# Kernel optimization log

Measured on AMD Instinct MI355X. Metric: run time of the kernel, lower is better.

The kernel has to match this reference:

```python
import jax, jax.numpy as jnp
import numpy as np

N_IMG = 1024
N_VIEWS = 90


def _bilinear(img, yi, xi):
    """Bilinear sample img at float coords (yi=row, xi=col); 0 outside (skimage warp cval=0)."""
    n = img.shape[0]
    y0 = jnp.floor(yi)
    x0 = jnp.floor(xi)
    wy = yi - y0
    wx = xi - x0
    y0i = y0.astype(jnp.int32)
    x0i = x0.astype(jnp.int32)

    def get(yy, xx):
        valid = (yy >= 0) & (yy < n) & (xx >= 0) & (xx < n)
        v = img[jnp.clip(yy, 0, n - 1), jnp.clip(xx, 0, n - 1)]
        return jnp.where(valid, v, jnp.zeros((), img.dtype))

    v00 = get(y0i, x0i)
    v01 = get(y0i, x0i + 1)
    v10 = get(y0i + 1, x0i)
    v11 = get(y0i + 1, x0i + 1)
    return (v00 * (1 - wy) * (1 - wx) + v01 * (1 - wy) * wx
            + v10 * wy * (1 - wx) + v11 * wy * wx)


def radon_jax(image, theta_deg):
    """skimage.transform.radon(image, theta, circle=True) equivalent.
    Rotate image by each angle (bilinear, about center = N//2, inverse map as in
    skimage warp) and sum over rows. Returns sinogram [N, n_angles]."""
    n = image.shape[0]
    center = n // 2
    ang = jnp.deg2rad(theta_deg.astype(image.dtype))
    cos_a = jnp.cos(ang)  # [A]
    sin_a = jnp.sin(ang)
    coords = jnp.arange(n, dtype=image.dtype)
    X, Y = jnp.meshgrid(coords, coords)  # X = col (x), Y = row (y), [N, N]

    def rotate_and_sum(ca, sa):
        # inverse map: src = R @ dst (homogeneous, (x, y) order) as in skimage radon
        x_in = ca * X + sa * Y - center * (ca + sa - 1)
        y_in = -sa * X + ca * Y - center * (ca - sa - 1)
        rotated = _bilinear(image, y_in, x_in)  # [N, N]
        return rotated.sum(axis=0)  # sum over rows -> projection [N]

    sino = jax.vmap(rotate_and_sum)(cos_a, sin_a)  # [A, N]
    return sino.T  # [N, A] to match skimage radon layout


def setup_inputs() -> dict:
    key = jax.random.key(0)
    k1, _ = jax.random.split(key)
    x = jax.random.normal(k1, (N_IMG, N_IMG), dtype=jnp.float32)
    theta = jnp.arange(N_VIEWS, dtype=jnp.float32) * 2.0  # 0..178 deg, 2-deg spacing
    return {"x": x, "theta": theta}


def reference(x, theta):
    return radon_jax(x, theta)
```

## Files before the change

kernel.cpp:

```cpp
#include <hip/hip_runtime.h>

#define N_IMG    1024
#define N_VIEWS  90
#define CENTER   512
#define NTHREADS 512
#define NWAVES   8
#define JOBS     4
#define PIT      96
#define BUFW     9088

typedef float v2f __attribute__((ext_vector_type(2)));

__device__ __forceinline__ void map_coords(float ca, float sa, float cx, float cy,
                                           float Xf, float Yf,
                                           float& x_in, float& y_in) {
    const float fx0 = fmaf(ca, Xf, cx);
    const float fy0 = fmaf(-sa, Xf, cy);
    x_in = fmaf(sa, Yf, fx0);
    y_in = fmaf(ca, Yf, fy0);
}

__device__ __forceinline__ void gload_lds4(const float* g, float* l) {
    __builtin_amdgcn_global_load_lds((const __attribute__((address_space(1))) void*)g,
                                     (__attribute__((address_space(3))) void*)l, 4, 0, 0);
}
__device__ __forceinline__ void gload_lds16(const float* g, float* l) {
    __builtin_amdgcn_global_load_lds((const __attribute__((address_space(1))) void*)g,
                                     (__attribute__((address_space(3))) void*)l, 16, 0, 0);
}

__global__ __launch_bounds__(256) void prep(const float* __restrict__ img,
                                            float* __restrict__ T,
                                            const float* __restrict__ theta,
                                            float* __restrict__ prm) {
    if (blockIdx.x == 256) {
        const int a = threadIdx.x;
        if (a < N_VIEWS) {
            const float ang = theta[a] * 0.017453292519943295f;
            double sd_, cd_;
            sincos((double)ang, &sd_, &cd_);
            const float s0 = (float)sd_, c0 = (float)cd_;
            const float cx0 = (float)CENTER * (1.0f - c0 - s0);
            const float cy0 = (float)CENTER * (1.0f - c0 + s0);
            float c, s, cx, cy, fl;
            if (fabsf(s0) > fabsf(c0)) {
                c = s0; s = -c0; cx = 1023.0f - cy0; cy = cx0; fl = 1.0f;
            } else {
                c = c0; s = s0;  cx = cx0;            cy = cy0;  fl = 0.0f;
            }
            float* p = prm + (a << 3);
            p[0] = c; p[1] = s; p[2] = cx; p[3] = cy; p[4] = fl;
        }
        return;
    }
    __shared__ float tile[64][65];
    const int t  = blockIdx.x, tr = t >> 4, tc = t & 15;
    const int tid = threadIdx.x, lane = tid & 63, w = tid >> 6;
    #pragma unroll
    for (int k = 0; k < 16; ++k) {
        const int row = (w << 4) + k;
        tile[row][lane] = img[(size_t)((tr << 6) + row) * N_IMG + (tc << 6) + lane];
    }
    __syncthreads();
    #pragma unroll
    for (int k = 0; k < 16; ++k) {
        const int j = (tc << 6) + (w << 4) + k;
        const int i = 1023 - ((tr << 6) + lane);
        T[(size_t)j * N_IMG + i] = tile[lane][(w << 4) + k];
    }
}

__global__ __launch_bounds__(NTHREADS, 8) void radon_fused(const float* __restrict__ img,
                                                           const float* __restrict__ Tbuf,
                                                           const float* __restrict__ theta,
                                                           const float* __restrict__ prm,
                                                           float* __restrict__ out,
                                                           int useT) {
    __shared__ float buf[BUFW];

    const int tx = blockIdx.x;
    const int q  = blockIdx.y;
    const int a  = blockIdx.z;
    const int X0 = tx * 64;
    const int Yq = q * (JOBS * 64);
    const int tid  = threadIdx.x;
    const int lane = tid & 63;
    const int wv   = tid >> 6;

    float c, s, cx, cy;
    const float* __restrict__ src;
    if (useT) {
        const float* p = prm + (a << 3);
        c = p[0]; s = p[1]; cx = p[2]; cy = p[3];
        src = (p[4] != 0.0f) ? Tbuf : img;
    } else {
        float s0, c0;
        __sincosf(theta[a] * 0.017453292519943295f, &s0, &c0);
        c = c0; s = s0;
        cx = (float)CENTER * (1.0f - c0 - s0);
        cy = (float)CENTER * (1.0f - c0 + s0);
        src = img;
    }

    const int jj = lane & (JOBS - 1);
    const float Yb = (float)(Yq + jj * 64);
    float x00, y00, x01, y01, x10, y10, x11, y11;
    map_coords(c, s, cx, cy, (float)X0,        Yb,        x00, y00);
    map_coords(c, s, cx, cy, (float)(X0 + 63), Yb,        x01, y01);
    map_coords(c, s, cx, cy, (float)X0,        Yb + 63.f, x10, y10);
    map_coords(c, s, cx, cy, (float)(X0 + 63), Yb + 63.f, x11, y11);
    const float xmin = fminf(fminf(x00, x01), fminf(x10, x11));
    const float xmax = fmaxf(fmaxf(x00, x01), fmaxf(x10, x11));
    const float ymin = fminf(fminf(y00, y01), fminf(y10, y11));
    const float ymax = fmaxf(fmaxf(y00, y01), fmaxf(y10, y11));

    const int ix0 = (int)floorf(xmin);
    const int ix1 = (int)floorf(xmax) + 1;
    const int iy0 = (int)floorf(ymin);
    const int iy1 = (int)floorf(ymax) + 1;

    const bool empty = (ix1 < 0) || (ix0 > N_IMG - 1) ||
                       (iy1 < 0) || (iy0 > N_IMG - 1);
    const bool interior = (ix0 >= 0) && (ix1 <= N_IMG - 1) &&
                          (iy0 >= 0) && (iy1 <= N_IMG - 1);
    const int winl = interior ? min(ix0 & ~3, N_IMG - PIT) : (ix0 & ~3);
    const int nrl  = iy1 - iy0 + 1;
    const int iy0l = iy0;
    const int fll  = empty ? 1 : (interior ? 2 : 0);

    const float Xf  = (float)(X0 + lane);
    const float bx  = fmaf(c, Xf, cx);
    const float by  = fmaf(-s, Xf, cy);
    const v2f s2 = {s, s}, c2 = {c, c};
    const v2f bx2 = {bx, bx}, by2 = {by, by};
    const v2f P2 = {(float)PIT, (float)PIT};
    float acc = 0.0f;

    for (int j = 0; j < JOBS; ++j) {
        const int win   = __shfl(winl, j);
        const int iyj   = __shfl(iy0l, j);
        const int nrows = __shfl(nrl,  j);
        const int fl    = __shfl(fll,  j);
        if (fl == 1) continue;

        if (fl & 2) {
            const int D = nrows * PIT;
            for (int o = wv * 256; o < D; o += NWAVES * 256) {
                const int d = o + 4 * lane;
                const int r = (unsigned)d / 96u;
                const int cc = d - r * 96;
                const int gr = min(iyj + r, N_IMG - 1);
                gload_lds16(src + (size_t)gr * N_IMG + win + cc, buf + o);
            }
        } else {
            for (int r = wv; r < nrows; r += NWAVES) {
                const int gy = iyj + r;
                const bool rok = ((unsigned)gy < (unsigned)N_IMG);
                const float* gp = src + (size_t)gy * N_IMG;
                float* l = buf + r * PIT;
                const int gx = win + lane;
                if (rok && (unsigned)gx < (unsigned)N_IMG) gload_lds4(gp + gx, l);
                else l[lane] = 0.0f;
                if (lane < 32) {
                    const int gx2 = gx + 64;
                    if (rok && (unsigned)gx2 < (unsigned)N_IMG) gload_lds4(gp + gx2, l + 64);
                    else l[64 + lane] = 0.0f;
                }
            }
        }
        __syncthreads();

        __builtin_amdgcn_s_setprio(1);
        const float Yw = (float)(Yq + j * 64 + wv * 8);
        const float basef = -(float)(iyj * PIT + win);
        const v2f b2 = {basef, basef};
        v2f Y2 = {Yw, Yw + 1.0f};
        const v2f two2 = {2.0f, 2.0f};
        v2f acc2 = {0.0f, 0.0f};
        #pragma unroll
        for (int p = 0; p < 4; ++p) {
            const v2f x2 = s2 * Y2 + bx2;
            const v2f y2 = c2 * Y2 + by2;
            const v2f x0f = {floorf(x2.x), floorf(x2.y)};
            const v2f y0f = {floorf(y2.x), floorf(y2.y)};
            const v2f wx = x2 - x0f;
            const v2f wy = y2 - y0f;
            const v2f lif = y0f * P2 + x0f + b2;
            const int li0 = (int)lif.x;
            const int li1 = (int)lif.y;
            const v2f t00 = {buf[li0],           buf[li1]};
            const v2f t01 = {buf[li0 + 1],       buf[li1 + 1]};
            const v2f t10 = {buf[li0 + PIT],     buf[li1 + PIT]};
            const v2f t11 = {buf[li0 + PIT + 1], buf[li1 + PIT + 1]};
            const v2f top = (t01 - t00) * wx + t00;
            const v2f bot = (t11 - t10) * wx + t10;
            acc2 += (bot - top) * wy + top;
            Y2 += two2;
        }
        acc += acc2.x + acc2.y;
        __builtin_amdgcn_s_setprio(0);

        __syncthreads();
    }

    buf[wv * 64 + lane] = acc;
    __syncthreads();
    if (wv == 0) {
        float ssum = 0.0f;
        #pragma unroll
        for (int w = 0; w < NWAVES; ++w) ssum += buf[w * 64 + lane];
        atomicAdd(&out[(size_t)(X0 + lane) * N_VIEWS + a], ssum);
    }
}

extern "C" void kernel_launch(void* const* d_in, const int* in_sizes, int n_in,
                              void* d_out, int out_size, void* d_ws, size_t ws_size,
                              hipStream_t stream) {
    const float* img   = (const float*)d_in[0];
    const float* theta = (const float*)d_in[1];
    float* out = (float*)d_out;

    const size_t tBytes = (size_t)N_IMG * N_IMG * sizeof(float);
    float* T   = (float*)d_ws;
    float* prm = (float*)((char*)d_ws + tBytes);
    const int useT = (ws_size >= tBytes + 4096) ? 1 : 0;

    (void)hipMemsetAsync(d_out, 0, (size_t)out_size * sizeof(float), stream);
    if (useT)
        prep<<<dim3(257), 256, 0, stream>>>(img, T, theta, prm);
    radon_fused<<<dim3(16, 4, N_VIEWS), NTHREADS, 0, stream>>>(img, useT ? T : img,
                                                               theta, prm, out, useT);
}
```

Measured before the change: 128.3 us.

## Double-buffer LDS staging with smaller row jobs to overlap loads and compute

Splits each block's rows into eight 32-row jobs and double-buffers the LDS window, so the next job's global-to-LDS copy is issued before the current job is interpolated. This removes one of the two barriers per job and aims to hide global load latency behind the bilinear gather work. In exchange the LDS footprint grows, launch bounds drop from 8 to 6 blocks per CU, the smaller windows carry proportionally more halo rows, and the row clamp in the interior path is replaced by clamping the last chunk's offset.

```diff
diff --git a/kernel.cpp b/kernel.cpp
--- a/kernel.cpp
+++ b/kernel.cpp
@@ -5,9 +5,9 @@
 #define CENTER   512
 #define NTHREADS 512
 #define NWAVES   8
-#define JOBS     4
+#define JOBS     8
 #define PIT      96
-#define BUFW     9088
+#define BUFP     6720
 
 typedef float v2f __attribute__((ext_vector_type(2)));
 
@@ -70,19 +70,19 @@
     }
 }
 
-__global__ __launch_bounds__(NTHREADS, 8) void radon_fused(const float* __restrict__ img,
+__global__ __launch_bounds__(NTHREADS, 6) void radon_fused(const float* __restrict__ img,
                                                            const float* __restrict__ Tbuf,
                                                            const float* __restrict__ theta,
                                                            const float* __restrict__ prm,
                                                            float* __restrict__ out,
                                                            int useT) {
-    __shared__ float buf[BUFW];
+    __shared__ float buf[2][BUFP];
 
     const int tx = blockIdx.x;
     const int q  = blockIdx.y;
     const int a  = blockIdx.z;
     const int X0 = tx * 64;
-    const int Yq = q * (JOBS * 64);
+    const int Yq = q * (JOBS * 32);
     const int tid  = threadIdx.x;
     const int lane = tid & 63;
     const int wv   = tid >> 6;
@@ -103,12 +103,12 @@
     }
 
     const int jj = lane & (JOBS - 1);
-    const float Yb = (float)(Yq + jj * 64);
+    const float Yb = (float)(Yq + jj * 32);
     float x00, y00, x01, y01, x10, y10, x11, y11;
     map_coords(c, s, cx, cy, (float)X0,        Yb,        x00, y00);
     map_coords(c, s, cx, cy, (float)(X0 + 63), Yb,        x01, y01);
-    map_coords(c, s, cx, cy, (float)X0,        Yb + 63.f, x10, y10);
-    map_coords(c, s, cx, cy, (float)(X0 + 63), Yb + 63.f, x11, y11);
+    map_coords(c, s, cx, cy, (float)X0,        Yb + 31.f, x10, y10);
+    map_coords(c, s, cx, cy, (float)(X0 + 63), Yb + 31.f, x11, y11);
     const float xmin = fminf(fminf(x00, x01), fminf(x10, x11));
     const float xmax = fmaxf(fmaxf(x00, x01), fmaxf(x10, x11));
     const float ymin = fminf(fminf(y00, y01), fminf(y10, y11));
@@ -136,28 +136,23 @@
     const v2f P2 = {(float)PIT, (float)PIT};
     float acc = 0.0f;
 
-    for (int j = 0; j < JOBS; ++j) {
-        const int win   = __shfl(winl, j);
-        const int iyj   = __shfl(iy0l, j);
-        const int nrows = __shfl(nrl,  j);
-        const int fl    = __shfl(fll,  j);
-        if (fl == 1) continue;
-
+    auto stage = [&](int win, int iyj, int nrows, int fl, float* dst) {
+        if (fl == 1) return;
         if (fl & 2) {
             const int D = nrows * PIT;
             for (int o = wv * 256; o < D; o += NWAVES * 256) {
-                const int d = o + 4 * lane;
+                const int oc = min(o, D - 256);
+                const int d = oc + 4 * lane;
                 const int r = (unsigned)d / 96u;
                 const int cc = d - r * 96;
-                const int gr = min(iyj + r, N_IMG - 1);
-                gload_lds16(src + (size_t)gr * N_IMG + win + cc, buf + o);
+                gload_lds16(src + (size_t)(iyj + r) * N_IMG + win + cc, dst + oc);
             }
         } else {
             for (int r = wv; r < nrows; r += NWAVES) {
                 const int gy = iyj + r;
                 const bool rok = ((unsigned)gy < (unsigned)N_IMG);
                 const float* gp = src + (size_t)gy * N_IMG;
-                float* l = buf + r * PIT;
+                float* l = dst + r * PIT;
                 const int gx = win + lane;
                 if (rok && (unsigned)gx < (unsigned)N_IMG) gload_lds4(gp + gx, l);
                 else l[lane] = 0.0f;
@@ -168,47 +163,62 @@
                 }
             }
         }
+    };
+
+    int wc = __shfl(winl, 0), yc = __shfl(iy0l, 0);
+    int nc = __shfl(nrl, 0),  fc = __shfl(fll, 0);
+    stage(wc, yc, nc, fc, buf[0]);
+    __syncthreads();
+
+    for (int j = 0; j < JOBS; ++j) {
+        int wn = wc, yn = yc, nn = nc, fn = fc;
+        if (j < JOBS - 1) {
+            wn = __shfl(winl, j + 1); yn = __shfl(iy0l, j + 1);
+            nn = __shfl(nrl,  j + 1); fn = __shfl(fll,  j + 1);
+            stage(wn, yn, nn, fn, buf[(j + 1) & 1]);
+        }
+        if (fc != 1) {
+            __builtin_amdgcn_s_setprio(1);
+            const float Yw = (float)(Yq + j * 32 + wv * 4);
+            const float basef = -(float)(yc * PIT + wc);
+            const v2f b2 = {basef, basef};
+            const float* bl = buf[j & 1];
+            v2f Y2 = {Yw, Yw + 1.0f};
+            const v2f two2 = {2.0f, 2.0f};
+            v2f acc2 = {0.0f, 0.0f};
+            #pragma unroll
+            for (int p = 0; p < 2; ++p) {
+                const v2f x2 = s2 * Y2 + bx2;
+                const v2f y2 = c2 * Y2 + by2;
+                const v2f x0f = {floorf(x2.x), floorf(x2.y)};
+                const v2f y0f = {floorf(y2.x), floorf(y2.y)};
+                const v2f wx = x2 - x0f;
+                const v2f wy = y2 - y0f;
+                const v2f lif = y0f * P2 + x0f + b2;
+                const int li0 = (int)lif.x;
+                const int li1 = (int)lif.y;
+                const v2f t00 = {bl[li0],           bl[li1]};
+                const v2f t01 = {bl[li0 + 1],       bl[li1 + 1]};
+                const v2f t10 = {bl[li0 + PIT],     bl[li1 + PIT]};
+                const v2f t11 = {bl[li0 + PIT + 1], bl[li1 + PIT + 1]};
+                const v2f top = (t01 - t00) * wx + t00;
+                const v2f bot = (t11 - t10) * wx + t10;
+                acc2 += (bot - top) * wy + top;
+                Y2 += two2;
+            }
+            acc += acc2.x + acc2.y;
+            __builtin_amdgcn_s_setprio(0);
+        }
         __syncthreads();
-
-        __builtin_amdgcn_s_setprio(1);
-        const float Yw = (float)(Yq + j * 64 + wv * 8);
-        const float basef = -(float)(iyj * PIT + win);
-        const v2f b2 = {basef, basef};
-        v2f Y2 = {Yw, Yw + 1.0f};
-        const v2f two2 = {2.0f, 2.0f};
-        v2f acc2 = {0.0f, 0.0f};
-        #pragma unroll
-        for (int p = 0; p < 4; ++p) {
-            const v2f x2 = s2 * Y2 + bx2;
-            const v2f y2 = c2 * Y2 + by2;
-            const v2f x0f = {floorf(x2.x), floorf(x2.y)};
-            const v2f y0f = {floorf(y2.x), floorf(y2.y)};
-            const v2f wx = x2 - x0f;
-            const v2f wy = y2 - y0f;
-            const v2f lif = y0f * P2 + x0f + b2;
-            const int li0 = (int)lif.x;
-            const int li1 = (int)lif.y;
-            const v2f t00 = {buf[li0],           buf[li1]};
-            const v2f t01 = {buf[li0 + 1],       buf[li1 + 1]};
-            const v2f t10 = {buf[li0 + PIT],     buf[li1 + PIT]};
-            const v2f t11 = {buf[li0 + PIT + 1], buf[li1 + PIT + 1]};
-            const v2f top = (t01 - t00) * wx + t00;
-            const v2f bot = (t11 - t10) * wx + t10;
-            acc2 += (bot - top) * wy + top;
-            Y2 += two2;
-        }
-        acc += acc2.x + acc2.y;
-        __builtin_amdgcn_s_setprio(0);
-
-        __syncthreads();
-    }
-
-    buf[wv * 64 + lane] = acc;
+        wc = wn; yc = yn; nc = nn; fc = fn;
+    }
+
+    buf[0][wv * 64 + lane] = acc;
     __syncthreads();
     if (wv == 0) {
         float ssum = 0.0f;
         #pragma unroll
-        for (int w = 0; w < NWAVES; ++w) ssum += buf[w * 64 + lane];
+        for (int w = 0; w < NWAVES; ++w) ssum += buf[0][w * 64 + lane];
         atomicAdd(&out[(size_t)(X0 + lane) * N_VIEWS + a], ssum);
     }
 }
```

Result: slower. 148.4 us (+15.7%).
